# Performance work log

Measured on AMD Instinct MI355X. Metric: run time of the kernel, lower is better.

The kernel has to match this reference:

```python
import jax, jax.numpy as jnp
import numpy as np

N, G, E = 100000, 32768, 1000000
F, H = 64, 64


def _mlp(x, w1, b1, w2, b2):
    # Linear -> SiLU -> Linear (matches nn.Sequential in the torch module)
    return jax.nn.silu(x @ w1 + b1) @ w2 + b2


def setup_inputs() -> dict:
    key = jax.random.key(0)
    ks = jax.random.split(key, 24)

    def lin(k, fan_in, fan_out):
        s = 1.0 / np.sqrt(fan_in)
        kw, kb = jax.random.split(k)
        w = jax.random.uniform(kw, (fan_in, fan_out), jnp.float32, -s, s)
        b = jax.random.uniform(kb, (fan_out,), jnp.float32, -s, s)
        return w, b

    node_w1, node_b1 = lin(ks[0], F, H)
    node_w2, node_b2 = lin(ks[1], H, H)
    edge_w1, edge_b1 = lin(ks[2], 6, H)
    edge_w2, edge_b2 = lin(ks[3], H, H)
    msg_w1, msg_b1 = lin(ks[4], 2 * H, H)
    msg_w2, msg_b2 = lin(ks[5], H, H)
    upd_w1, upd_b1 = lin(ks[6], H, H)
    upd_w2, upd_b2 = lin(ks[7], H, H)

    return {
        "node_features": jax.random.normal(ks[8], (N, F), jnp.float32),
        "node_pos": jax.random.normal(ks[9], (N, 3), jnp.float32),
        "grid_pos": jax.random.normal(ks[10], (G, 3), jnp.float32),
        "orientations": jax.random.normal(ks[11], (N, 3, 3), jnp.float32),
        "edge_index": jnp.stack([
            jax.random.randint(ks[12], (E,), 0, N),
            jax.random.randint(ks[13], (E,), 0, G),
        ]),
        "node_w1": node_w1, "node_b1": node_b1, "node_w2": node_w2, "node_b2": node_b2,
        "edge_w1": edge_w1, "edge_b1": edge_b1, "edge_w2": edge_w2, "edge_b2": edge_b2,
        "msg_w1": msg_w1, "msg_b1": msg_b1, "msg_w2": msg_w2, "msg_b2": msg_b2,
        "upd_w1": upd_w1, "upd_b1": upd_b1, "upd_w2": upd_w2, "upd_b2": upd_b2,
    }


def reference(node_features, node_pos, grid_pos, orientations, edge_index,
              node_w1, node_b1, node_w2, node_b2,
              edge_w1, edge_b1, edge_w2, edge_b2,
              msg_w1, msg_b1, msg_w2, msg_b2,
              upd_w1, upd_b1, upd_w2, upd_b2):
    source, target = edge_index[0], edge_index[1]
    num_grid = grid_pos.shape[0]

    # node MLP
    h_node = _mlp(node_features, node_w1, node_b1, node_w2, node_b2)  # [N,H]

    # per-edge message with orientation-aware projection
    pos_s = node_pos[source]                 # [E,3]
    rel = grid_pos[target] - pos_s           # [E,3]
    # bmm(rel[:,None,:], R[source]).squeeze(1) == einsum ei,eij->ej
    trel = jnp.einsum("ei,eij->ej", rel, orientations[source])
    edge_attr = jnp.concatenate([pos_s, trel], axis=-1)        # [E,6]
    e_feat = _mlp(edge_attr, edge_w1, edge_b1, edge_w2, edge_b2)
    msg_in = jnp.concatenate([h_node[source], e_feat], axis=-1)  # [E,2H]
    messages = _mlp(msg_in, msg_w1, msg_b1, msg_w2, msg_b2)      # [E,H]

    # scatter-mean into grid buckets (mask out-of-range targets)
    valid = (target >= 0) & (target < num_grid)
    idx = jnp.where(valid, target, 0)
    msg_masked = jnp.where(valid[:, None], messages, 0.0)
    sums = jax.ops.segment_sum(msg_masked, idx, num_segments=num_grid)
    cnts = jax.ops.segment_sum(valid.astype(jnp.float32), idx, num_segments=num_grid)
    grid_feat = sums / jnp.maximum(cnts, 1.0)[:, None]

    return _mlp(grid_feat, upd_w1, upd_b1, upd_w2, upd_b2)  # [G,H]
```

## Files before the change

### kernel.cpp

```cpp
#include <hip/hip_runtime.h>
#include <cstdint>

typedef __attribute__((ext_vector_type(8))) short short8;
typedef __attribute__((ext_vector_type(4))) float f32x4;
typedef unsigned short u16;

__device__ __forceinline__ float b2f(u16 u) {
  union { unsigned int i; float f; } v; v.i = ((unsigned int)u) << 16; return v.f;
}
__device__ __forceinline__ u16 f2b(float f) {
  union { float f; unsigned int i; } v; v.f = f;
  unsigned int x = v.i;
  return (u16)((x + 0x7fffu + ((x >> 16) & 1u)) >> 16);
}
__device__ __forceinline__ float silu_f(float x) { return x / (1.0f + __expf(-x)); }

__device__ __forceinline__ float loadF(const void* p, long i, int isf32) {
  if (isf32) return ((const float*)p)[i];
  return b2f(((const u16*)p)[i]);
}

struct Ptrs { const void* p[20]; int n[20]; };

#define FW_NW1 0
#define FW_NW2 4096
#define FW_UW1 8192
#define FW_UW2 12288
#define FW_EW1 16384
#define FW_NB1 16768
#define FW_NB2 16832
#define FW_UB1 16896
#define FW_UB2 16960
#define FW_EB1 17024
#define FW_EB2 17088
#define FW_MB1 17152
#define FW_MB2 17216
#define FW_TOTAL 17280

#define IMG_EW2 0
#define IMG_MW1 4608
#define IMG_MW2 13312
#define IMG_TOTAL 17920

__global__ __launch_bounds__(256) void detect_k(Ptrs a, int* flags) {
  int j = blockIdx.x;
  const u16* q = (const u16*)a.p[j];
  int n = a.n[j];
  int m = n < 4096 ? n : 4096;
  int cnt = 0;
  for (int i = threadIdx.x; i < m; i += 256) {
    unsigned e = (q[i] >> 7) & 0xffu;
    if (e >= 0xC0u) cnt++;
  }
  __shared__ int tot;
  if (threadIdx.x == 0) tot = 0;
  __syncthreads();
  if (cnt) atomicAdd(&tot, cnt);
  __syncthreads();
  if (threadIdx.x == 0) flags[j] = (tot >= 2) ? 1 : 0;
}

__global__ __launch_bounds__(256) void prep_k(Ptrs a, const int* flags,
                                              u16* img, float* fw) {
  int i = blockIdx.x * 256 + threadIdx.x;
  if (i < IMG_TOTAL) {
    u16 val = 0;
    if (i < IMG_MW1) {
      int nn = i / 72, k = i % 72;
      if (k < 64) val = f2b(loadF(a.p[10], (long)k * 64 + nn, flags[10]));
    } else if (i < IMG_MW2) {
      int t2 = i - IMG_MW1; int nn = t2 / 136, k = t2 % 136;
      if (k < 128) val = f2b(loadF(a.p[12], (long)k * 64 + nn, flags[12]));
    } else {
      int t2 = i - IMG_MW2; int nn = t2 / 72, k = t2 % 72;
      if (k < 64) val = f2b(loadF(a.p[14], (long)k * 64 + nn, flags[14]));
    }
    img[i] = val;
  } else if (i < IMG_TOTAL + FW_TOTAL) {
    int j = i - IMG_TOTAL;
    float v;
    if (j < 4096)            v = loadF(a.p[4],  j,          flags[4]);
    else if (j < 8192)       v = loadF(a.p[6],  j - 4096,   flags[6]);
    else if (j < 12288)      v = loadF(a.p[16], j - 8192,   flags[16]);
    else if (j < 16384)      v = loadF(a.p[18], j - 12288,  flags[18]);
    else if (j < 16768)      v = loadF(a.p[8],  j - 16384,  flags[8]);
    else {
      int b = j - 16768; int seg = b >> 6, c = b & 63;
      const void* bp; int bf;
      switch (seg) {
        case 0: bp = a.p[5];  bf = flags[5];  break;
        case 1: bp = a.p[7];  bf = flags[7];  break;
        case 2: bp = a.p[17]; bf = flags[17]; break;
        case 3: bp = a.p[19]; bf = flags[19]; break;
        case 4: bp = a.p[9];  bf = flags[9];  break;
        case 5: bp = a.p[11]; bf = flags[11]; break;
        case 6: bp = a.p[13]; bf = flags[13]; break;
        default: bp = a.p[15]; bf = flags[15]; break;
      }
      v = loadF(bp, c, bf);
    }
    fw[j] = v;
  }
}

__global__ __launch_bounds__(256) void hist_k(const int* __restrict__ eidx,
                                              int* __restrict__ cnt, long E, int G) {
  long i = (long)blockIdx.x * 256 + threadIdx.x;
  const long stride = (long)gridDim.x * 256;
  for (; i < E; i += stride) {
    int tg = eidx[E + i];
    if (tg >= 0 && tg < G) atomicAdd(&cnt[tg], 1);
  }
}

__global__ __launch_bounds__(1024) void scan_k(const int* __restrict__ cnt,
                                               int* __restrict__ cursor,
                                               int* __restrict__ evp, int G) {
  __shared__ int sd[1024];
  __shared__ int carry;
  const int t = threadIdx.x;
  if (t == 0) carry = 0;
  __syncthreads();
  for (int c0 = 0; c0 < G; c0 += 1024) {
    int i = c0 + t;
    int v = (i < G) ? cnt[i] : 0;
    sd[t] = v;
    __syncthreads();
    for (int off = 1; off < 1024; off <<= 1) {
      int x = (t >= off) ? sd[t - off] : 0;
      __syncthreads();
      sd[t] += x;
      __syncthreads();
    }
    int excl = sd[t] - v + carry;
    if (i < G) cursor[i] = excl;
    int tot = sd[1023];
    __syncthreads();
    if (t == 0) carry += tot;
    __syncthreads();
  }
  if (t == 0) *evp = carry;
}

__global__ __launch_bounds__(256) void scat_k(const int* __restrict__ eidx,
                                              int* __restrict__ cursor,
                                              unsigned int* __restrict__ pkS,
                                              long E, int G) {
  long i = (long)blockIdx.x * 256 + threadIdx.x;
  const long stride = (long)gridDim.x * 256;
  for (; i < E; i += stride) {
    int tg = eidx[E + i];
    if (tg >= 0 && tg < G) {
      int s = eidx[i];
      int p = atomicAdd(&cursor[tg], 1);
      pkS[p] = (unsigned int)s | ((unsigned int)tg << 17);
    }
  }
}

__global__ __launch_bounds__(256) void node_mlp(
    const void* x, const int* flags, const float* fw, u16* out, int nrows)
{
  __shared__ float xs[64][68];
  __shared__ float w1s[64][68];
  __shared__ float w2s[64][68];
  __shared__ float b1s[64];
  __shared__ float b2s[64];
  const int t = threadIdx.x;
  const int xf = flags[0];
  const long rbase = (long)blockIdx.x * 64;
  for (int i = t; i < 4096; i += 256) {
    int k = i >> 6, cc = i & 63;
    w1s[k][cc] = fw[FW_NW1 + i];
    w2s[k][cc] = fw[FW_NW2 + i];
  }
  if (t < 64) { b1s[t] = fw[FW_NB1 + t]; b2s[t] = fw[FW_NB2 + t]; }
  {
    int row = t >> 2, ch = t & 3;
    long rg = rbase + row;
    if (rg < nrows) {
      if (xf) {
        const float* xp = (const float*)x + rg * 64 + ch * 16;
#pragma unroll
        for (int m = 0; m < 16; ++m) xs[row][ch * 16 + m] = xp[m];
      } else {
        const u16* xp = (const u16*)x + rg * 64 + ch * 16;
#pragma unroll
        for (int m = 0; m < 16; ++m) xs[row][ch * 16 + m] = b2f(xp[m]);
      }
    } else {
#pragma unroll
      for (int m = 0; m < 16; ++m) xs[row][ch * 16 + m] = 0.f;
    }
  }
  __syncthreads();
  const int r0 = (t >> 4) * 4, c0 = (t & 15) * 4;
  float acc[4][4];
#pragma unroll
  for (int i = 0; i < 4; ++i)
#pragma unroll
    for (int j = 0; j < 4; ++j) acc[i][j] = b1s[c0 + j];
  for (int k = 0; k < 64; ++k) {
    float w0 = w1s[k][c0], w1v = w1s[k][c0 + 1], w2v = w1s[k][c0 + 2], w3v = w1s[k][c0 + 3];
#pragma unroll
    for (int i = 0; i < 4; ++i) {
      float a = xs[r0 + i][k];
      acc[i][0] = fmaf(a, w0, acc[i][0]);
      acc[i][1] = fmaf(a, w1v, acc[i][1]);
      acc[i][2] = fmaf(a, w2v, acc[i][2]);
      acc[i][3] = fmaf(a, w3v, acc[i][3]);
    }
  }
  __syncthreads();
#pragma unroll
  for (int i = 0; i < 4; ++i)
#pragma unroll
    for (int j = 0; j < 4; ++j) xs[r0 + i][c0 + j] = silu_f(acc[i][j]);
  __syncthreads();
  float acc2[4][4];
#pragma unroll
  for (int i = 0; i < 4; ++i)
#pragma unroll
    for (int j = 0; j < 4; ++j) acc2[i][j] = b2s[c0 + j];
  for (int k = 0; k < 64; ++k) {
    float w0 = w2s[k][c0], w1v = w2s[k][c0 + 1], w2v = w2s[k][c0 + 2], w3v = w2s[k][c0 + 3];
#pragma unroll
    for (int i = 0; i < 4; ++i) {
      float a = xs[r0 + i][k];
      acc2[i][0] = fmaf(a, w0, acc2[i][0]);
      acc2[i][1] = fmaf(a, w1v, acc2[i][1]);
      acc2[i][2] = fmaf(a, w2v, acc2[i][2]);
      acc2[i][3] = fmaf(a, w3v, acc2[i][3]);
    }
  }
#pragma unroll
  for (int i = 0; i < 4; ++i) {
    long rg = rbase + r0 + i;
    if (rg < nrows) {
#pragma unroll
      for (int j = 0; j < 4; ++j) out[rg * 64 + c0 + j] = f2b(acc2[i][j]);
    }
  }
}

#define ETILES 4

__global__ __launch_bounds__(256, 3) void edge_kernel(
    const void* node_pos, const void* grid_pos, const void* orient,
    const unsigned int* __restrict__ pkS, const int* __restrict__ evp,
    const u16* __restrict__ h_node, const u16* __restrict__ img,
    const float* __restrict__ fw, const int* __restrict__ flags,
    float* __restrict__ sums, int G)
{
  __shared__ __align__(16) u16 hA[64][136];
  __shared__ __align__(16) u16 ef1[64][72];
  __shared__ __align__(16) float msgf[64][66];
  __shared__ float eaf[64][6];
  __shared__ float w1e[6][64];
  __shared__ float biasE[4][64];
  __shared__ int src_s[64];
  __shared__ int tgt_s[64];

  const int t = threadIdx.x;
  const int pf = flags[1], gf = flags[2], of = flags[3];
  const int Ev = *evp;

  for (int i = t; i < 384; i += 256) w1e[i / 64][i % 64] = fw[FW_EW1 + i];
  { int seg = t >> 6, cc = t & 63; biasE[seg][cc] = fw[FW_EB1 + seg * 64 + cc]; }

  const int lane = t & 63, w = t >> 6;
  const int q = lane >> 4, c = lane & 15;
  const int m0 = w * 16;
  const u16* wE2 = img + IMG_EW2;
  const u16* wM1 = img + IMG_MW1;
  const u16* wM2 = img + IMG_MW2;
  const f32x4 z = {0.f, 0.f, 0.f, 0.f};

  for (int tile = 0; tile < ETILES; ++tile) {
    long base = ((long)blockIdx.x * ETILES + tile) * 64;
    if (base >= Ev) break;
    __syncthreads();
    if (t < 64) {
      long eg = base + t;
      int s, tg;
      if (eg < Ev) {
        unsigned int pk = pkS[eg];
        s = (int)(pk & 0x1FFFFu);
        tg = (int)(pk >> 17);
      } else { s = 0; tg = -1; }
      src_s[t] = s;
      tgt_s[t] = tg;
      int tgc = (tg >= 0) ? tg : 0;
      float ps[3], rel[3], tr[3];
#pragma unroll
      for (int i = 0; i < 3; ++i) {
        ps[i] = loadF(node_pos, (long)s * 3 + i, pf);
        rel[i] = loadF(grid_pos, (long)tgc * 3 + i, gf) - ps[i];
      }
#pragma unroll
      for (int j = 0; j < 3; ++j) tr[j] = 0.f;
#pragma unroll
      for (int i = 0; i < 3; ++i)
#pragma unroll
        for (int j = 0; j < 3; ++j)
          tr[j] = fmaf(rel[i], loadF(orient, (long)s * 9 + i * 3 + j, of), tr[j]);
      eaf[t][0] = ps[0]; eaf[t][1] = ps[1]; eaf[t][2] = ps[2];
      eaf[t][3] = tr[0]; eaf[t][4] = tr[1]; eaf[t][5] = tr[2];
    }
    __syncthreads();
    {
      int e = t >> 2, ch = t & 3;
      const u16* hp = h_node + (long)src_s[e] * 64 + ch * 16;
      short8 v0 = *(const short8*)hp;
      short8 v1 = *(const short8*)(hp + 8);
      *(short8*)&hA[e][ch * 16] = v0;
      *(short8*)&hA[e][ch * 16 + 8] = v1;
    }
    __syncthreads();

    {
      int e = t >> 2, c0 = (t & 3) * 16;
      float a0 = eaf[e][0], a1 = eaf[e][1], a2 = eaf[e][2];
      float a3 = eaf[e][3], a4 = eaf[e][4], a5 = eaf[e][5];
      __align__(16) u16 tmp[16];
#pragma unroll
      for (int j = 0; j < 16; ++j) {
        int cc = c0 + j;
        float acc = biasE[0][cc];
        acc = fmaf(a0, w1e[0][cc], acc);
        acc = fmaf(a1, w1e[1][cc], acc);
        acc = fmaf(a2, w1e[2][cc], acc);
        acc = fmaf(a3, w1e[3][cc], acc);
        acc = fmaf(a4, w1e[4][cc], acc);
        acc = fmaf(a5, w1e[5][cc], acc);
        tmp[j] = f2b(silu_f(acc));
      }
      *(short8*)&ef1[e][c0] = *(const short8*)tmp;
      *(short8*)&ef1[e][c0 + 8] = *(const short8*)(tmp + 8);
    }
    __syncthreads();
    {
      short8 a0 = *(const short8*)&ef1[m0 + c][q * 8];
      short8 a1 = *(const short8*)&ef1[m0 + c][32 + q * 8];
#pragma unroll
      for (int nt = 0; nt < 4; ++nt) {
        short8 b0 = *(const short8*)&wE2[(nt * 16 + c) * 72 + q * 8];
        short8 b1v = *(const short8*)&wE2[(nt * 16 + c) * 72 + 32 + q * 8];
        f32x4 acc = __builtin_amdgcn_mfma_f32_16x16x32_bf16(a0, b0, z, 0, 0, 0);
        acc = __builtin_amdgcn_mfma_f32_16x16x32_bf16(a1, b1v, acc, 0, 0, 0);
#pragma unroll
        for (int r = 0; r < 4; ++r) {
          int row = m0 + q * 4 + r, col = nt * 16 + c;
          hA[row][64 + col] = f2b(acc[r] + biasE[1][col]);
        }
      }
    }
    __syncthreads();
    {
      short8 a0 = *(const short8*)&hA[m0 + c][q * 8];
      short8 a1 = *(const short8*)&hA[m0 + c][32 + q * 8];
      short8 a2 = *(const short8*)&hA[m0 + c][64 + q * 8];
      short8 a3 = *(const short8*)&hA[m0 + c][96 + q * 8];
#pragma unroll
      for (int nt = 0; nt < 4; ++nt) {
        const u16* wp = &wM1[(nt * 16 + c) * 136];
        f32x4 acc = __builtin_amdgcn_mfma_f32_16x16x32_bf16(a0, *(const short8*)(wp + q * 8), z, 0, 0, 0);
        acc = __builtin_amdgcn_mfma_f32_16x16x32_bf16(a1, *(const short8*)(wp + 32 + q * 8), acc, 0, 0, 0);
        acc = __builtin_amdgcn_mfma_f32_16x16x32_bf16(a2, *(const short8*)(wp + 64 + q * 8), acc, 0, 0, 0);
        acc = __builtin_amdgcn_mfma_f32_16x16x32_bf16(a3, *(const short8*)(wp + 96 + q * 8), acc, 0, 0, 0);
#pragma unroll
        for (int r = 0; r < 4; ++r) {
          int row = m0 + q * 4 + r, col = nt * 16 + c;
          ef1[row][col] = f2b(silu_f(acc[r] + biasE[2][col]));
        }
      }
    }
    __syncthreads();
    {
      short8 a0 = *(const short8*)&ef1[m0 + c][q * 8];
      short8 a1 = *(const short8*)&ef1[m0 + c][32 + q * 8];
#pragma unroll
      for (int nt = 0; nt < 4; ++nt) {
        short8 b0 = *(const short8*)&wM2[(nt * 16 + c) * 72 + q * 8];
        short8 b1v = *(const short8*)&wM2[(nt * 16 + c) * 72 + 32 + q * 8];
        f32x4 acc = __builtin_amdgcn_mfma_f32_16x16x32_bf16(a0, b0, z, 0, 0, 0);
        acc = __builtin_amdgcn_mfma_f32_16x16x32_bf16(a1, b1v, acc, 0, 0, 0);
#pragma unroll
        for (int r = 0; r < 4; ++r) {
          int row = m0 + q * 4 + r, col = nt * 16 + c;
          msgf[row][col] = acc[r] + biasE[3][col];
        }
      }
    }
    __syncthreads();
    {
      int col = lane;
      int r0 = w * 16;
      int cur = tgt_s[r0];
      float run = msgf[r0][col];
      bool lopen = (r0 == 0) ? true : (tgt_s[r0 - 1] == cur);
#pragma unroll
      for (int r2 = 1; r2 < 16; ++r2) {
        int r = r0 + r2;
        int tg = tgt_s[r];
        float v = msgf[r][col];
        if (tg == cur) {
          run += v;
        } else {
          if (cur >= 0) {
            if (lopen) unsafeAtomicAdd(&sums[(long)cur * 64 + col], run);
            else sums[(long)cur * 64 + col] = run;
          }
          cur = tg; run = v; lopen = false;
        }
      }
      bool ropen = (r0 + 16 >= 64) ? true : (tgt_s[r0 + 16] == cur);
      if (cur >= 0) {
        if (lopen || ropen) unsafeAtomicAdd(&sums[(long)cur * 64 + col], run);
        else sums[(long)cur * 64 + col] = run;
      }
    }
  }
}

__global__ __launch_bounds__(256) void upd_mlp(
    const float* __restrict__ sums, const int* __restrict__ cnt,
    const float* __restrict__ fw, float* __restrict__ out, int nrows)
{
  __shared__ float xs[64][68];
  __shared__ float w1s[64][68];
  __shared__ float w2s[64][68];
  __shared__ float b1s[64];
  __shared__ float b2s[64];
  const int t = threadIdx.x;
  const long rbase = (long)blockIdx.x * 64;
  for (int i = t; i < 4096; i += 256) {
    int k = i >> 6, cc = i & 63;
    w1s[k][cc] = fw[FW_UW1 + i];
    w2s[k][cc] = fw[FW_UW2 + i];
  }
  if (t < 64) { b1s[t] = fw[FW_UB1 + t]; b2s[t] = fw[FW_UB2 + t]; }
  {
    int row = t >> 2, ch = t & 3;
    long rg = rbase + row;
    if (rg < nrows) {
      float inv = 1.0f / fmaxf((float)cnt[rg], 1.0f);
      const float* p = sums + rg * 64 + ch * 16;
#pragma unroll
      for (int m = 0; m < 16; ++m) xs[row][ch * 16 + m] = p[m] * inv;
    } else {
#pragma unroll
      for (int m = 0; m < 16; ++m) xs[row][ch * 16 + m] = 0.f;
    }
  }
  __syncthreads();
  const int r0 = (t >> 4) * 4, c0 = (t & 15) * 4;
  float acc[4][4];
#pragma unroll
  for (int i = 0; i < 4; ++i)
#pragma unroll
    for (int j = 0; j < 4; ++j) acc[i][j] = b1s[c0 + j];
  for (int k = 0; k < 64; ++k) {
    float w0 = w1s[k][c0], w1v = w1s[k][c0 + 1], w2v = w1s[k][c0 + 2], w3v = w1s[k][c0 + 3];
#pragma unroll
    for (int i = 0; i < 4; ++i) {
      float a = xs[r0 + i][k];
      acc[i][0] = fmaf(a, w0, acc[i][0]);
      acc[i][1] = fmaf(a, w1v, acc[i][1]);
      acc[i][2] = fmaf(a, w2v, acc[i][2]);
      acc[i][3] = fmaf(a, w3v, acc[i][3]);
    }
  }
  __syncthreads();
#pragma unroll
  for (int i = 0; i < 4; ++i)
#pragma unroll
    for (int j = 0; j < 4; ++j) xs[r0 + i][c0 + j] = silu_f(acc[i][j]);
  __syncthreads();
  float acc2[4][4];
#pragma unroll
  for (int i = 0; i < 4; ++i)
#pragma unroll
    for (int j = 0; j < 4; ++j) acc2[i][j] = b2s[c0 + j];
  for (int k = 0; k < 64; ++k) {
    float w0 = w2s[k][c0], w1v = w2s[k][c0 + 1], w2v = w2s[k][c0 + 2], w3v = w2s[k][c0 + 3];
#pragma unroll
    for (int i = 0; i < 4; ++i) {
      float a = xs[r0 + i][k];
      acc2[i][0] = fmaf(a, w0, acc2[i][0]);
      acc2[i][1] = fmaf(a, w1v, acc2[i][1]);
      acc2[i][2] = fmaf(a, w2v, acc2[i][2]);
      acc2[i][3] = fmaf(a, w3v, acc2[i][3]);
    }
  }
#pragma unroll
  for (int i = 0; i < 4; ++i) {
    long rg = rbase + r0 + i;
    if (rg < nrows) {
#pragma unroll
      for (int j = 0; j < 4; ++j) out[rg * 64 + c0 + j] = acc2[i][j];
    }
  }
}

extern "C" void kernel_launch(void* const* d_in, const int* in_sizes, int n_in,
                              void* d_out, int out_size, void* d_ws, size_t ws_size,
                              hipStream_t stream) {
  const int N = in_sizes[1] / 3;
  const int G = in_sizes[2] / 3;
  const long E = (long)in_sizes[4] / 2;

  char* ws = (char*)d_ws;
  int* flags = (int*)ws;
  int* evp = flags + 24;
  float* sums = (float*)(ws + 256);
  size_t off = 256 + (size_t)G * 256;
  int* cnt = (int*)(ws + off);     off += (size_t)G * 4;
  int* cursor = (int*)(ws + off);  off += (size_t)G * 4;
  unsigned int* pkS = (unsigned int*)(ws + off); off += (size_t)E * 4;
  u16* h_node = (u16*)(ws + off);  off += (size_t)N * 128;
  u16* img = (u16*)(ws + off);     off += (size_t)IMG_TOTAL * 2;
  float* fw = (float*)(ws + off);

  hipMemsetAsync(ws, 0, 256 + (size_t)G * 256 + (size_t)G * 4, stream);

  Ptrs a;
  const int map[20] = {0,1,2,3, 5,6,7,8, 9,10,11,12, 13,14,15,16, 17,18,19,20};
  for (int i = 0; i < 20; ++i) { a.p[i] = d_in[map[i]]; a.n[i] = in_sizes[map[i]]; }

  detect_k<<<20, 256, 0, stream>>>(a, flags);
  prep_k<<<(IMG_TOTAL + FW_TOTAL + 255) / 256, 256, 0, stream>>>(a, flags, img, fw);
  hist_k<<<1024, 256, 0, stream>>>((const int*)d_in[4], cnt, E, G);
  scan_k<<<1, 1024, 0, stream>>>(cnt, cursor, evp, G);
  node_mlp<<<(N + 63) / 64, 256, 0, stream>>>(d_in[0], flags, fw, h_node, N);
  scat_k<<<1024, 256, 0, stream>>>((const int*)d_in[4], cursor, pkS, E, G);
  edge_kernel<<<(int)((E + ETILES * 64 - 1) / (ETILES * 64)), 256, 0, stream>>>(
      d_in[1], d_in[2], d_in[3], pkS, evp, h_node, img, fw, flags,
      sums, G);
  upd_mlp<<<(G + 63) / 64, 256, 0, stream>>>(sums, cnt, fw, (float*)d_out, G);
}
```

Measured before the change: 529.3 us.

## Fuse preprocessing kernels, parallelize scan, prefetch edge tiles, raise edge occupancy

Result: slower. 545.6 us (+3.1%).

```diff
diff --git a/kernel.cpp b/kernel.cpp
--- a/kernel.cpp
+++ b/kernel.cpp
@@ -1,4 +1,5 @@
 #include <hip/hip_runtime.h>
+#include <hip/hip_bf16.h>
 #include <cstdint>
 
 typedef __attribute__((ext_vector_type(8))) short short8;
@@ -9,9 +10,8 @@
   union { unsigned int i; float f; } v; v.i = ((unsigned int)u) << 16; return v.f;
 }
 __device__ __forceinline__ u16 f2b(float f) {
-  union { float f; unsigned int i; } v; v.f = f;
-  unsigned int x = v.i;
-  return (u16)((x + 0x7fffu + ((x >> 16) & 1u)) >> 16);
+  __hip_bfloat16 h = __float2bfloat16(f);
+  union { __hip_bfloat16 h; u16 u; } v; v.h = h; return v.u;
 }
 __device__ __forceinline__ float silu_f(float x) { return x / (1.0f + __expf(-x)); }
 
@@ -20,7 +20,15 @@
   return b2f(((const u16*)p)[i]);
 }
 
-struct Ptrs { const void* p[20]; int n[20]; };
+__device__ __forceinline__ int detect1(const void* p, int n) {
+  const u16* q = (const u16*)p;
+  int m = n < 512 ? n : 512;
+  int h = 0;
+  for (int k = 0; k < m; ++k) h += (((q[k] >> 7) & 0xffu) >= 0xC0u) ? 1 : 0;
+  return h >= 2;
+}
+
+struct Ptrs { const void* p[20]; };
 
 #define FW_NW1 0
 #define FW_NW2 4096
@@ -42,132 +50,96 @@
 #define IMG_MW2 13312
 #define IMG_TOTAL 17920
 
-__global__ __launch_bounds__(256) void detect_k(Ptrs a, int* flags) {
-  int j = blockIdx.x;
-  const u16* q = (const u16*)a.p[j];
-  int n = a.n[j];
-  int m = n < 4096 ? n : 4096;
-  int cnt = 0;
-  for (int i = threadIdx.x; i < m; i += 256) {
-    unsigned e = (q[i] >> 7) & 0xffu;
-    if (e >= 0xC0u) cnt++;
-  }
-  __shared__ int tot;
-  if (threadIdx.x == 0) tot = 0;
-  __syncthreads();
-  if (cnt) atomicAdd(&tot, cnt);
-  __syncthreads();
-  if (threadIdx.x == 0) flags[j] = (tot >= 2) ? 1 : 0;
-}
-
-__global__ __launch_bounds__(256) void prep_k(Ptrs a, const int* flags,
-                                              u16* img, float* fw) {
-  int i = blockIdx.x * 256 + threadIdx.x;
+#define PREP_BLOCKS 138
+#define HIST_BLOCKS 1024
+
+__global__ __launch_bounds__(256) void prep_hist_k(Ptrs a, u16* img, float* fw,
+                                                   const int* __restrict__ eidx,
+                                                   int* __restrict__ cnt,
+                                                   long E, int G) {
+  const int t = threadIdx.x;
+  if ((int)blockIdx.x >= PREP_BLOCKS) {
+    long i = (long)(blockIdx.x - PREP_BLOCKS) * 256 + t;
+    const long stride = (long)HIST_BLOCKS * 256;
+    for (; i < E; i += stride) {
+      int tg = eidx[E + i];
+      if (tg >= 0 && tg < G) atomicAdd(&cnt[tg], 1);
+    }
+    return;
+  }
+  int i = blockIdx.x * 256 + t;
   if (i < IMG_TOTAL) {
+    const void* bp; int n; long si; bool real;
+    if (i < IMG_MW1) { int nn = i / 72, k = i % 72; bp = a.p[10]; n = 4096; real = k < 64; si = (long)k * 64 + nn; }
+    else if (i < IMG_MW2) { int t2 = i - IMG_MW1; int nn = t2 / 136, k = t2 % 136; bp = a.p[12]; n = 8192; real = k < 128; si = (long)k * 64 + nn; }
+    else { int t2 = i - IMG_MW2; int nn = t2 / 72, k = t2 % 72; bp = a.p[14]; n = 4096; real = k < 64; si = (long)k * 64 + nn; }
     u16 val = 0;
-    if (i < IMG_MW1) {
-      int nn = i / 72, k = i % 72;
-      if (k < 64) val = f2b(loadF(a.p[10], (long)k * 64 + nn, flags[10]));
-    } else if (i < IMG_MW2) {
-      int t2 = i - IMG_MW1; int nn = t2 / 136, k = t2 % 136;
-      if (k < 128) val = f2b(loadF(a.p[12], (long)k * 64 + nn, flags[12]));
-    } else {
-      int t2 = i - IMG_MW2; int nn = t2 / 72, k = t2 % 72;
-      if (k < 64) val = f2b(loadF(a.p[14], (long)k * 64 + nn, flags[14]));
-    }
+    if (real) { int isf = detect1(bp, n); val = f2b(loadF(bp, si, isf)); }
     img[i] = val;
   } else if (i < IMG_TOTAL + FW_TOTAL) {
     int j = i - IMG_TOTAL;
-    float v;
-    if (j < 4096)            v = loadF(a.p[4],  j,          flags[4]);
-    else if (j < 8192)       v = loadF(a.p[6],  j - 4096,   flags[6]);
-    else if (j < 12288)      v = loadF(a.p[16], j - 8192,   flags[16]);
-    else if (j < 16384)      v = loadF(a.p[18], j - 12288,  flags[18]);
-    else if (j < 16768)      v = loadF(a.p[8],  j - 16384,  flags[8]);
+    const void* bp; int n; long si;
+    if (j < 4096)       { bp = a.p[4];  n = 4096; si = j; }
+    else if (j < 8192)  { bp = a.p[6];  n = 4096; si = j - 4096; }
+    else if (j < 12288) { bp = a.p[16]; n = 4096; si = j - 8192; }
+    else if (j < 16384) { bp = a.p[18]; n = 4096; si = j - 12288; }
+    else if (j < 16768) { bp = a.p[8];  n = 384;  si = j - 16384; }
     else {
-      int b = j - 16768; int seg = b >> 6, c = b & 63;
-      const void* bp; int bf;
+      int b = j - 16768; int seg = b >> 6; si = b & 63; n = 64;
       switch (seg) {
-        case 0: bp = a.p[5];  bf = flags[5];  break;
-        case 1: bp = a.p[7];  bf = flags[7];  break;
-        case 2: bp = a.p[17]; bf = flags[17]; break;
-        case 3: bp = a.p[19]; bf = flags[19]; break;
-        case 4: bp = a.p[9];  bf = flags[9];  break;
-        case 5: bp = a.p[11]; bf = flags[11]; break;
-        case 6: bp = a.p[13]; bf = flags[13]; break;
-        default: bp = a.p[15]; bf = flags[15]; break;
-      }
-      v = loadF(bp, c, bf);
-    }
-    fw[j] = v;
-  }
-}
-
-__global__ __launch_bounds__(256) void hist_k(const int* __restrict__ eidx,
-                                              int* __restrict__ cnt, long E, int G) {
-  long i = (long)blockIdx.x * 256 + threadIdx.x;
-  const long stride = (long)gridDim.x * 256;
-  for (; i < E; i += stride) {
-    int tg = eidx[E + i];
-    if (tg >= 0 && tg < G) atomicAdd(&cnt[tg], 1);
-  }
-}
-
-__global__ __launch_bounds__(1024) void scan_k(const int* __restrict__ cnt,
-                                               int* __restrict__ cursor,
-                                               int* __restrict__ evp, int G) {
-  __shared__ int sd[1024];
-  __shared__ int carry;
-  const int t = threadIdx.x;
-  if (t == 0) carry = 0;
-  __syncthreads();
-  for (int c0 = 0; c0 < G; c0 += 1024) {
-    int i = c0 + t;
-    int v = (i < G) ? cnt[i] : 0;
-    sd[t] = v;
-    __syncthreads();
-    for (int off = 1; off < 1024; off <<= 1) {
-      int x = (t >= off) ? sd[t - off] : 0;
-      __syncthreads();
-      sd[t] += x;
-      __syncthreads();
-    }
-    int excl = sd[t] - v + carry;
-    if (i < G) cursor[i] = excl;
-    int tot = sd[1023];
-    __syncthreads();
-    if (t == 0) carry += tot;
-    __syncthreads();
-  }
-  if (t == 0) *evp = carry;
-}
-
-__global__ __launch_bounds__(256) void scat_k(const int* __restrict__ eidx,
-                                              int* __restrict__ cursor,
-                                              unsigned int* __restrict__ pkS,
-                                              long E, int G) {
-  long i = (long)blockIdx.x * 256 + threadIdx.x;
-  const long stride = (long)gridDim.x * 256;
-  for (; i < E; i += stride) {
-    int tg = eidx[E + i];
-    if (tg >= 0 && tg < G) {
-      int s = eidx[i];
-      int p = atomicAdd(&cursor[tg], 1);
-      pkS[p] = (unsigned int)s | ((unsigned int)tg << 17);
-    }
-  }
-}
-
-__global__ __launch_bounds__(256) void node_mlp(
-    const void* x, const int* flags, const float* fw, u16* out, int nrows)
+        case 0: bp = a.p[5];  break;
+        case 1: bp = a.p[7];  break;
+        case 2: bp = a.p[17]; break;
+        case 3: bp = a.p[19]; break;
+        case 4: bp = a.p[9];  break;
+        case 5: bp = a.p[11]; break;
+        case 6: bp = a.p[13]; break;
+        default: bp = a.p[15]; break;
+      }
+    }
+    int isf = detect1(bp, n);
+    fw[j] = loadF(bp, si, isf);
+  }
+}
+
+__global__ __launch_bounds__(256) void node_scan_k(
+    const void* x, const float* __restrict__ fw, u16* __restrict__ out, int nrows,
+    const int* __restrict__ cnt, int* __restrict__ cursor, int* __restrict__ bsum,
+    int G, int nodeBlocks)
 {
   __shared__ float xs[64][68];
   __shared__ float w1s[64][68];
   __shared__ float w2s[64][68];
   __shared__ float b1s[64];
   __shared__ float b2s[64];
+  __shared__ int sd2[256];
+  __shared__ int xdet;
   const int t = threadIdx.x;
-  const int xf = flags[0];
+
+  if ((int)blockIdx.x >= nodeBlocks) {
+    int b2 = blockIdx.x - nodeBlocks;
+    int i = b2 * 256 + t;
+    int v = (i < G) ? cnt[i] : 0;
+    sd2[t] = v;
+    __syncthreads();
+    for (int off = 1; off < 256; off <<= 1) {
+      int x2 = (t >= off) ? sd2[t - off] : 0;
+      __syncthreads();
+      sd2[t] += x2;
+      __syncthreads();
+    }
+    if (i < G) cursor[i] = sd2[t] - v;
+    if (t == 255) bsum[b2] = sd2[255];
+    return;
+  }
+  if (t == 0) xdet = 0;
+  __syncthreads();
+  {
+    const u16* q = (const u16*)x;
+    int c = 0;
+    for (int i = t; i < 4096; i += 256) c += (((q[i] >> 7) & 0xffu) >= 0xC0u) ? 1 : 0;
+    if (c) atomicAdd(&xdet, c);
+  }
   const long rbase = (long)blockIdx.x * 64;
   for (int i = t; i < 4096; i += 256) {
     int k = i >> 6, cc = i & 63;
@@ -175,6 +147,8 @@
     w2s[k][cc] = fw[FW_NW2 + i];
   }
   if (t < 64) { b1s[t] = fw[FW_NB1 + t]; b2s[t] = fw[FW_NB2 + t]; }
+  __syncthreads();
+  const int xf = xdet >= 2;
   {
     int row = t >> 2, ch = t & 3;
     long rg = rbase + row;
@@ -204,11 +178,11 @@
     float w0 = w1s[k][c0], w1v = w1s[k][c0 + 1], w2v = w1s[k][c0 + 2], w3v = w1s[k][c0 + 3];
 #pragma unroll
     for (int i = 0; i < 4; ++i) {
-      float a = xs[r0 + i][k];
-      acc[i][0] = fmaf(a, w0, acc[i][0]);
-      acc[i][1] = fmaf(a, w1v, acc[i][1]);
-      acc[i][2] = fmaf(a, w2v, acc[i][2]);
-      acc[i][3] = fmaf(a, w3v, acc[i][3]);
+      float av = xs[r0 + i][k];
+      acc[i][0] = fmaf(av, w0, acc[i][0]);
+      acc[i][1] = fmaf(av, w1v, acc[i][1]);
+      acc[i][2] = fmaf(av, w2v, acc[i][2]);
+      acc[i][3] = fmaf(av, w3v, acc[i][3]);
     }
   }
   __syncthreads();
@@ -226,11 +200,11 @@
     float w0 = w2s[k][c0], w1v = w2s[k][c0 + 1], w2v = w2s[k][c0 + 2], w3v = w2s[k][c0 + 3];
 #pragma unroll
     for (int i = 0; i < 4; ++i) {
-      float a = xs[r0 + i][k];
-      acc2[i][0] = fmaf(a, w0, acc2[i][0]);
-      acc2[i][1] = fmaf(a, w1v, acc2[i][1]);
-      acc2[i][2] = fmaf(a, w2v, acc2[i][2]);
-      acc2[i][3] = fmaf(a, w3v, acc2[i][3]);
+      float av = xs[r0 + i][k];
+      acc2[i][0] = fmaf(av, w0, acc2[i][0]);
+      acc2[i][1] = fmaf(av, w1v, acc2[i][1]);
+      acc2[i][2] = fmaf(av, w2v, acc2[i][2]);
+      acc2[i][3] = fmaf(av, w3v, acc2[i][3]);
     }
   }
 #pragma unroll
@@ -243,30 +217,75 @@
   }
 }
 
+__global__ __launch_bounds__(256) void scat_k(const int* __restrict__ eidx,
+                                              int* __restrict__ cursor,
+                                              const int* __restrict__ bsum,
+                                              unsigned int* __restrict__ pkS,
+                                              int* __restrict__ evp,
+                                              long E, int G, int NB2) {
+  __shared__ int bo[256];
+  const int t = threadIdx.x;
+  int v = (t < NB2) ? bsum[t] : 0;
+  bo[t] = v;
+  __syncthreads();
+  for (int off = 1; off < 256; off <<= 1) {
+    int x2 = (t >= off) ? bo[t - off] : 0;
+    __syncthreads();
+    bo[t] += x2;
+    __syncthreads();
+  }
+  if (blockIdx.x == 0 && t == 0) *evp = bo[NB2 - 1];
+  int excl = bo[t] - v;
+  __syncthreads();
+  bo[t] = excl;
+  __syncthreads();
+  long i = (long)blockIdx.x * 256 + t;
+  const long stride = (long)gridDim.x * 256;
+  for (; i < E; i += stride) {
+    int tg = eidx[E + i];
+    if (tg >= 0 && tg < G) {
+      int s = eidx[i];
+      int p = atomicAdd(&cursor[tg], 1) + bo[tg >> 8];
+      pkS[p] = (unsigned int)s | ((unsigned int)tg << 17);
+    }
+  }
+}
+
 #define ETILES 4
 
-__global__ __launch_bounds__(256, 3) void edge_kernel(
+__global__ __launch_bounds__(256, 5) void edge_kernel(
     const void* node_pos, const void* grid_pos, const void* orient,
     const unsigned int* __restrict__ pkS, const int* __restrict__ evp,
     const u16* __restrict__ h_node, const u16* __restrict__ img,
-    const float* __restrict__ fw, const int* __restrict__ flags,
+    const float* __restrict__ fw,
     float* __restrict__ sums, int G)
 {
   __shared__ __align__(16) u16 hA[64][136];
   __shared__ __align__(16) u16 ef1[64][72];
-  __shared__ __align__(16) float msgf[64][66];
   __shared__ float eaf[64][6];
   __shared__ float w1e[6][64];
   __shared__ float biasE[4][64];
-  __shared__ int src_s[64];
   __shared__ int tgt_s[64];
+  __shared__ int det[3];
+  float (*msgf)[66] = (float (*)[66])&hA[0][0];
 
   const int t = threadIdx.x;
-  const int pf = flags[1], gf = flags[2], of = flags[3];
-  const int Ev = *evp;
-
+  if (t < 3) det[t] = 0;
+  __syncthreads();
+  {
+    int grp = t >> 6;
+    if (grp < 3) {
+      const u16* q = (const u16*)(grp == 0 ? node_pos : grp == 1 ? grid_pos : orient);
+      int c = 0, l = t & 63;
+      for (int i = l; i < 2048; i += 64) c += (((q[i] >> 7) & 0xffu) >= 0xC0u) ? 1 : 0;
+      if (c) atomicAdd(&det[grp], c);
+    }
+  }
   for (int i = t; i < 384; i += 256) w1e[i / 64][i % 64] = fw[FW_EW1 + i];
   { int seg = t >> 6, cc = t & 63; biasE[seg][cc] = fw[FW_EB1 + seg * 64 + cc]; }
+  __syncthreads();
+  const int pf = det[0] >= 2, gf = det[1] >= 2, of = det[2] >= 2;
+  const int Ev = *evp;
 
   const int lane = t & 63, w = t >> 6;
   const int q = lane >> 4, c = lane & 15;
@@ -276,20 +295,24 @@
   const u16* wM2 = img + IMG_MW2;
   const f32x4 z = {0.f, 0.f, 0.f, 0.f};
 
-  for (int tile = 0; tile < ETILES; ++tile) {
-    long base = ((long)blockIdx.x * ETILES + tile) * 64;
-    if (base >= Ev) break;
-    __syncthreads();
+  short8 hv0, hv1;
+  int my_tg = -1;
+  float g0 = 0, g1 = 0, g2 = 0, g3 = 0, g4 = 0, g5 = 0;
+
+  auto prefetch = [&](long base) {
+    {
+      long eg = base + (t >> 2);
+      int s = 0;
+      if (eg < Ev) s = (int)(pkS[eg] & 0x1FFFFu);
+      const u16* hp = h_node + (long)s * 64 + (t & 3) * 16;
+      hv0 = *(const short8*)hp;
+      hv1 = *(const short8*)(hp + 8);
+    }
     if (t < 64) {
       long eg = base + t;
-      int s, tg;
-      if (eg < Ev) {
-        unsigned int pk = pkS[eg];
-        s = (int)(pk & 0x1FFFFu);
-        tg = (int)(pk >> 17);
-      } else { s = 0; tg = -1; }
-      src_s[t] = s;
-      tgt_s[t] = tg;
+      int s = 0, tg = -1;
+      if (eg < Ev) { unsigned int pk = pkS[eg]; s = (int)(pk & 0x1FFFFu); tg = (int)(pk >> 17); }
+      my_tg = tg;
       int tgc = (tg >= 0) ? tg : 0;
       float ps[3], rel[3], tr[3];
 #pragma unroll
@@ -304,18 +327,28 @@
 #pragma unroll
         for (int j = 0; j < 3; ++j)
           tr[j] = fmaf(rel[i], loadF(orient, (long)s * 9 + i * 3 + j, of), tr[j]);
-      eaf[t][0] = ps[0]; eaf[t][1] = ps[1]; eaf[t][2] = ps[2];
-      eaf[t][3] = tr[0]; eaf[t][4] = tr[1]; eaf[t][5] = tr[2];
-    }
-    __syncthreads();
+      g0 = ps[0]; g1 = ps[1]; g2 = ps[2]; g3 = tr[0]; g4 = tr[1]; g5 = tr[2];
+    }
+  };
+
+  const long blk0 = (long)blockIdx.x * ETILES * 64;
+  prefetch(blk0);
+
+  for (int tile = 0; tile < ETILES; ++tile) {
+    long base = blk0 + (long)tile * 64;
+    if (base >= Ev) break;
+    __syncthreads();
+    if (t < 64) {
+      tgt_s[t] = my_tg;
+      eaf[t][0] = g0; eaf[t][1] = g1; eaf[t][2] = g2;
+      eaf[t][3] = g3; eaf[t][4] = g4; eaf[t][5] = g5;
+    }
     {
       int e = t >> 2, ch = t & 3;
-      const u16* hp = h_node + (long)src_s[e] * 64 + ch * 16;
-      short8 v0 = *(const short8*)hp;
-      short8 v1 = *(const short8*)(hp + 8);
-      *(short8*)&hA[e][ch * 16] = v0;
-      *(short8*)&hA[e][ch * 16 + 8] = v1;
-    }
+      *(short8*)&hA[e][ch * 16] = hv0;
+      *(short8*)&hA[e][ch * 16 + 8] = hv1;
+    }
+    prefetch(base + 64);
     __syncthreads();
 
     {
@@ -464,11 +497,11 @@
     float w0 = w1s[k][c0], w1v = w1s[k][c0 + 1], w2v = w1s[k][c0 + 2], w3v = w1s[k][c0 + 3];
 #pragma unroll
     for (int i = 0; i < 4; ++i) {
-      float a = xs[r0 + i][k];
-      acc[i][0] = fmaf(a, w0, acc[i][0]);
-      acc[i][1] = fmaf(a, w1v, acc[i][1]);
-      acc[i][2] = fmaf(a, w2v, acc[i][2]);
-      acc[i][3] = fmaf(a, w3v, acc[i][3]);
+      float av = xs[r0 + i][k];
+      acc[i][0] = fmaf(av, w0, acc[i][0]);
+      acc[i][1] = fmaf(av, w1v, acc[i][1]);
+      acc[i][2] = fmaf(av, w2v, acc[i][2]);
+      acc[i][3] = fmaf(av, w3v, acc[i][3]);
     }
   }
   __syncthreads();
@@ -486,11 +519,11 @@
     float w0 = w2s[k][c0], w1v = w2s[k][c0 + 1], w2v = w2s[k][c0 + 2], w3v = w2s[k][c0 + 3];
 #pragma unroll
     for (int i = 0; i < 4; ++i) {
-      float a = xs[r0 + i][k];
-      acc2[i][0] = fmaf(a, w0, acc2[i][0]);
-      acc2[i][1] = fmaf(a, w1v, acc2[i][1]);
-      acc2[i][2] = fmaf(a, w2v, acc2[i][2]);
-      acc2[i][3] = fmaf(a, w3v, acc2[i][3]);
+      float av = xs[r0 + i][k];
+      acc2[i][0] = fmaf(av, w0, acc2[i][0]);
+      acc2[i][1] = fmaf(av, w1v, acc2[i][1]);
+      acc2[i][2] = fmaf(av, w2v, acc2[i][2]);
+      acc2[i][3] = fmaf(av, w3v, acc2[i][3]);
     }
   }
 #pragma unroll
@@ -509,33 +542,33 @@
   const int N = in_sizes[1] / 3;
   const int G = in_sizes[2] / 3;
   const long E = (long)in_sizes[4] / 2;
+  const int NB2 = (G + 255) / 256;
+  const int nodeBlocks = (N + 63) / 64;
 
   char* ws = (char*)d_ws;
-  int* flags = (int*)ws;
-  int* evp = flags + 24;
-  float* sums = (float*)(ws + 256);
-  size_t off = 256 + (size_t)G * 256;
+  float* sums = (float*)ws;
+  size_t off = (size_t)G * 256;
   int* cnt = (int*)(ws + off);     off += (size_t)G * 4;
   int* cursor = (int*)(ws + off);  off += (size_t)G * 4;
+  int* bsum = (int*)(ws + off);    off += 1024;
+  int* evp = (int*)(ws + off);     off += 256;
   unsigned int* pkS = (unsigned int*)(ws + off); off += (size_t)E * 4;
   u16* h_node = (u16*)(ws + off);  off += (size_t)N * 128;
   u16* img = (u16*)(ws + off);     off += (size_t)IMG_TOTAL * 2;
   float* fw = (float*)(ws + off);
 
-  hipMemsetAsync(ws, 0, 256 + (size_t)G * 256 + (size_t)G * 4, stream);
+  hipMemsetAsync(ws, 0, (size_t)G * 260, stream);
 
   Ptrs a;
   const int map[20] = {0,1,2,3, 5,6,7,8, 9,10,11,12, 13,14,15,16, 17,18,19,20};
-  for (int i = 0; i < 20; ++i) { a.p[i] = d_in[map[i]]; a.n[i] = in_sizes[map[i]]; }
-
-  detect_k<<<20, 256, 0, stream>>>(a, flags);
-  prep_k<<<(IMG_TOTAL + FW_TOTAL + 255) / 256, 256, 0, stream>>>(a, flags, img, fw);
-  hist_k<<<1024, 256, 0, stream>>>((const int*)d_in[4], cnt, E, G);
-  scan_k<<<1, 1024, 0, stream>>>(cnt, cursor, evp, G);
-  node_mlp<<<(N + 63) / 64, 256, 0, stream>>>(d_in[0], flags, fw, h_node, N);
-  scat_k<<<1024, 256, 0, stream>>>((const int*)d_in[4], cursor, pkS, E, G);
+  for (int i = 0; i < 20; ++i) a.p[i] = d_in[map[i]];
+
+  prep_hist_k<<<PREP_BLOCKS + HIST_BLOCKS, 256, 0, stream>>>(
+      a, img, fw, (const int*)d_in[4], cnt, E, G);
+  node_scan_k<<<nodeBlocks + NB2, 256, 0, stream>>>(
+      d_in[0], fw, h_node, N, cnt, cursor, bsum, G, nodeBlocks);
+  scat_k<<<1024, 256, 0, stream>>>((const int*)d_in[4], cursor, bsum, pkS, evp, E, G, NB2);
   edge_kernel<<<(int)((E + ETILES * 64 - 1) / (ETILES * 64)), 256, 0, stream>>>(
-      d_in[1], d_in[2], d_in[3], pkS, evp, h_node, img, fw, flags,
-      sums, G);
+      d_in[1], d_in[2], d_in[3], pkS, evp, h_node, img, fw, sums, G);
   upd_mlp<<<(G + 63) / 64, 256, 0, stream>>>(sums, cnt, fw, (float*)d_out, G);
 }
```
